# Kernel tuning notes

Hardware: AMD Instinct MI355X
Metric: run time of the kernel (lower is better)

## Reference

```python
import jax, jax.numpy as jnp
import numpy as np

L, B, T, D = 4, 32, 2048, 100


def setup_inputs() -> dict:
    key = jax.random.key(0)
    k1, k2 = jax.random.split(key)
    h = jax.random.normal(k1, (L, B, T, D), dtype=jnp.float32)
    old_h = jax.random.normal(k2, (L, B, T, D), dtype=jnp.float32)
    layer_weights = jnp.ones((L,), dtype=jnp.float32)
    class_weights = jnp.ones((D,), dtype=jnp.float32)
    return {"h": h, "old_h": old_h, "layer_weights": layer_weights, "class_weights": class_weights}


def reference(h, old_h, layer_weights, class_weights):
    # h, old_h: [L, B, T, D]. Softmax / log_softmax are over the T axis
    # (dim=-1 of h[..., c] which is [B, T]).
    logq = jax.nn.log_softmax(h, axis=2)        # student log-probs  [L,B,T,D]
    logp = jax.nn.log_softmax(old_h, axis=2)    # teacher log-probs  [L,B,T,D]
    p = jnp.exp(logp)                            # teacher probs
    # KL(p || q) per (layer, class), batchmean reduction: sum over (B,T) / B
    kl_lc = jnp.sum(p * (logp - logq), axis=(1, 2)) / jnp.float32(B)  # [L, D]
    lw = jax.nn.softmax(layer_weights)           # [L]
    cw = jax.nn.softmax(class_weights)           # [D]
    loss = jnp.einsum('l,ld,d->', lw, kl_lc, cw)
    return loss
```

## Files before the change

### kernel.cpp

```cpp
#include <hip/hip_runtime.h>

constexpr int kL = 4;
constexpr int kB = 32;
constexpr int kT = 2048;
constexpr int kD = 100;
constexpr int kD4 = kD / 4;
constexpr int kCH = 16;
constexpr int kTSUB = kT / kCH;
constexpr int kROWS = kL * kB * kD;

__global__ __launch_bounds__(256) void kl_partial(
    const float4* __restrict__ h4, const float4* __restrict__ oh4,
    float* __restrict__ wsp, float* __restrict__ wsq, float* __restrict__ ww) {
  const int lb = blockIdx.x >> 4;
  const int chunk = blockIdx.x & 15;
  const int tid = threadIdx.x;
  const int ty = tid >> 6;
  const int lane = tid & 63;
  const int half = lane / kD4;
  const int d4 = lane - half * kD4;
  const bool active = (lane < 2 * kD4);

  float4 sp = {0.f, 0.f, 0.f, 0.f};
  float4 sq = {0.f, 0.f, 0.f, 0.f};
  float4 w  = {0.f, 0.f, 0.f, 0.f};

  if (active) {
    const int row0 = chunk * kTSUB + ty * 2 + half;
    const size_t b4 = ((size_t)lb * kT + row0) * kD4 + d4;
    const float4* __restrict__ hp = h4 + b4;
    const float4* __restrict__ op = oh4 + b4;
    for (int i = 0; i < 4; ++i) {
      const float4 h0 = hp[0];
      const float4 o0 = op[0];
      const float4 h1 = hp[200];
      const float4 o1 = op[200];
      const float4 h2 = hp[400];
      const float4 o2 = op[400];
      const float4 h3 = hp[600];
      const float4 o3 = op[600];
      hp += 800; op += 800;
      {
        const float a = __expf(o0.x), b = __expf(o0.y), c = __expf(o0.z), d = __expf(o0.w);
        sp.x += a; sp.y += b; sp.z += c; sp.w += d;
        sq.x += __expf(h0.x); sq.y += __expf(h0.y); sq.z += __expf(h0.z); sq.w += __expf(h0.w);
        w.x += a * (o0.x - h0.x); w.y += b * (o0.y - h0.y);
        w.z += c * (o0.z - h0.z); w.w += d * (o0.w - h0.w);
      }
      {
        const float a = __expf(o1.x), b = __expf(o1.y), c = __expf(o1.z), d = __expf(o1.w);
        sp.x += a; sp.y += b; sp.z += c; sp.w += d;
        sq.x += __expf(h1.x); sq.y += __expf(h1.y); sq.z += __expf(h1.z); sq.w += __expf(h1.w);
        w.x += a * (o1.x - h1.x); w.y += b * (o1.y - h1.y);
        w.z += c * (o1.z - h1.z); w.w += d * (o1.w - h1.w);
      }
      {
        const float a = __expf(o2.x), b = __expf(o2.y), c = __expf(o2.z), d = __expf(o2.w);
        sp.x += a; sp.y += b; sp.z += c; sp.w += d;
        sq.x += __expf(h2.x); sq.y += __expf(h2.y); sq.z += __expf(h2.z); sq.w += __expf(h2.w);
        w.x += a * (o2.x - h2.x); w.y += b * (o2.y - h2.y);
        w.z += c * (o2.z - h2.z); w.w += d * (o2.w - h2.w);
      }
      {
        const float a = __expf(o3.x), b = __expf(o3.y), c = __expf(o3.z), d = __expf(o3.w);
        sp.x += a; sp.y += b; sp.z += c; sp.w += d;
        sq.x += __expf(h3.x); sq.y += __expf(h3.y); sq.z += __expf(h3.z); sq.w += __expf(h3.w);
        w.x += a * (o3.x - h3.x); w.y += b * (o3.y - h3.y);
        w.z += c * (o3.z - h3.z); w.w += d * (o3.w - h3.w);
      }
    }
  }

  __shared__ float red[256][12];
  {
    float* r = red[tid];
    r[0] = sp.x; r[1] = sp.y; r[2]  = sp.z; r[3]  = sp.w;
    r[4] = sq.x; r[5] = sq.y; r[6]  = sq.z; r[7]  = sq.w;
    r[8] = w.x;  r[9] = w.y;  r[10] = w.z;  r[11] = w.w;
  }
  __syncthreads();
  if (tid < kD) {
    const int dd4 = tid >> 2, j = tid & 3;
    float asp = 0.f, asq = 0.f, aw = 0.f;
#pragma unroll
    for (int g = 0; g < 4; ++g) {
#pragma unroll
      for (int hh = 0; hh < 2; ++hh) {
        const float* s = red[g * 64 + hh * kD4 + dd4];
        asp += s[j]; asq += s[4 + j]; aw += s[8 + j];
      }
    }
    const int idx = lb * kD + tid;
    atomicAdd(&wsp[idx], asp);
    atomicAdd(&wsq[idx], asq);
    atomicAdd(&ww[idx],  aw);
  }
}

__global__ __launch_bounds__(256) void kl_reduce(
    const float* __restrict__ wsp, const float* __restrict__ wsq,
    const float* __restrict__ ww, const float* __restrict__ lwin,
    const float* __restrict__ cwin, float* __restrict__ acc) {
  __shared__ float lw[kL];
  __shared__ float cw[kD];
  __shared__ float sred[256];
  const int tid = threadIdx.x;

  if (tid == 0) {
    float m = lwin[0];
    for (int i = 1; i < kL; ++i) m = fmaxf(m, lwin[i]);
    float e[kL], s = 0.f;
    for (int i = 0; i < kL; ++i) { e[i] = __expf(lwin[i] - m); s += e[i]; }
    const float inv = 1.0f / s;
    for (int i = 0; i < kL; ++i) lw[i] = e[i] * inv;
  }
  if (tid == 64) {
    float m = cwin[0];
    for (int i = 1; i < kD; ++i) m = fmaxf(m, cwin[i]);
    float s = 0.f;
    for (int i = 0; i < kD; ++i) { const float e = __expf(cwin[i] - m); cw[i] = e; s += e; }
    const float inv = 1.0f / s;
    for (int i = 0; i < kD; ++i) cw[i] *= inv;
  }
  __syncthreads();

  const int r = blockIdx.x * 256 + tid;
  const int l = r / (kB * kD);
  const int d = r % kD;
  const float spv = wsp[r], sqv = wsq[r], wv = ww[r];
  const float val = wv / spv - __logf(spv) + __logf(sqv);
  sred[tid] = lw[l] * cw[d] * val;
  __syncthreads();
  for (int s = 128; s > 0; s >>= 1) {
    if (tid < s) sred[tid] += sred[tid + s];
    __syncthreads();
  }
  if (tid == 0) atomicAdd(acc, sred[0]);
}

__global__ void kl_write(const float* __restrict__ acc, float* __restrict__ out) {
  out[0] = acc[0] / (float)kB;
}

extern "C" void kernel_launch(void* const* d_in, const int* in_sizes, int n_in,
                              void* d_out, int out_size, void* d_ws, size_t ws_size,
                              hipStream_t stream) {
  const float* h    = (const float*)d_in[0];
  const float* oh   = (const float*)d_in[1];
  const float* lwin = (const float*)d_in[2];
  const float* cwin = (const float*)d_in[3];

  float* wsp = (float*)d_ws;
  float* wsq = wsp + kROWS;
  float* ww  = wsq + kROWS;
  float* acc = ww + kROWS;
  hipMemsetAsync(d_ws, 0, ((size_t)3 * kROWS + 1) * sizeof(float), stream);

  kl_partial<<<kL * kB * kCH, 256, 0, stream>>>(
      (const float4*)h, (const float4*)oh, wsp, wsq, ww);
  kl_reduce<<<kROWS / 256, 256, 0, stream>>>(wsp, wsq, ww, lwin, cwin, acc);
  kl_write<<<1, 1, 0, stream>>>(acc, (float*)d_out);
}
```

Measured before the change: 241.8 us.

## Replace atomic accumulation and memset with deterministic per-block partials and tree reduction

When the workspace is large enough, each partial block writes its per-class sums to its own slot instead of using global atomics, which removes the memset launch and atomic contention. A per-(layer,batch) reduce kernel then sums the 16 chunks, and a small wave-shuffle kernel produces the final scalar. The streaming loop is also fully unrolled, with all loads grouped ahead of a scheduling barrier to raise memory-level parallelism. The old atomic path stays as a fallback, at the cost of a larger workspace requirement.

```diff
diff --git a/kernel.cpp b/kernel.cpp
--- a/kernel.cpp
+++ b/kernel.cpp
@@ -7,69 +7,163 @@
 constexpr int kD4 = kD / 4;
 constexpr int kCH = 16;
 constexpr int kTSUB = kT / kCH;
-constexpr int kROWS = kL * kB * kD;
-
-__global__ __launch_bounds__(256) void kl_partial(
-    const float4* __restrict__ h4, const float4* __restrict__ oh4,
-    float* __restrict__ wsp, float* __restrict__ wsq, float* __restrict__ ww) {
-  const int lb = blockIdx.x >> 4;
-  const int chunk = blockIdx.x & 15;
-  const int tid = threadIdx.x;
+constexpr int kLB = kL * kB;
+constexpr int kROWS = kLB * kD;
+constexpr int kNBLK = kLB * kCH;
+
+#define KL_PAIR(hx, ox)                                                      \
+  {                                                                          \
+    const float ea = __expf(ox.x), eb = __expf(ox.y), ec = __expf(ox.z),     \
+                ed = __expf(ox.w);                                           \
+    sp.x += ea; sp.y += eb; sp.z += ec; sp.w += ed;                          \
+    sq.x += __expf(hx.x); sq.y += __expf(hx.y);                              \
+    sq.z += __expf(hx.z); sq.w += __expf(hx.w);                              \
+    w.x += ea * (ox.x - hx.x); w.y += eb * (ox.y - hx.y);                    \
+    w.z += ec * (ox.z - hx.z); w.w += ed * (ox.w - hx.w);                    \
+  }
+
+__device__ __forceinline__ void stream_slab(const float4* __restrict__ hp,
+                                            const float4* __restrict__ op,
+                                            float4& sp, float4& sq, float4& w) {
+#pragma unroll
+  for (int i = 0; i < 4; ++i) {
+    const float4 h0 = hp[0];
+    const float4 h1 = hp[200];
+    const float4 h2 = hp[400];
+    const float4 h3 = hp[600];
+    const float4 o0 = op[0];
+    const float4 o1 = op[200];
+    const float4 o2 = op[400];
+    const float4 o3 = op[600];
+    hp += 800; op += 800;
+    __builtin_amdgcn_sched_barrier(0);
+    KL_PAIR(h0, o0)
+    KL_PAIR(h1, o1)
+    KL_PAIR(h2, o2)
+    KL_PAIR(h3, o3)
+  }
+}
+
+template <int PASS>
+__device__ __forceinline__ void partial_body(const float4* __restrict__ h4,
+                                             const float4* __restrict__ oh4,
+                                             float4& sp, float4& sq, float4& w,
+                                             int lb, int chunk, int tid) {
   const int ty = tid >> 6;
   const int lane = tid & 63;
   const int half = lane / kD4;
   const int d4 = lane - half * kD4;
   const bool active = (lane < 2 * kD4);
+  if (active) {
+    const int row0 = chunk * kTSUB + ty * 2 + half;
+    const size_t b4 = ((size_t)lb * kT + row0) * kD4 + d4;
+    stream_slab(h4 + b4, oh4 + b4, sp, sq, w);
+  }
+}
+
+__global__ __launch_bounds__(256) void kl_partial_na(
+    const float4* __restrict__ h4, const float4* __restrict__ oh4,
+    float* __restrict__ psp, float* __restrict__ psq, float* __restrict__ pw) {
+  const int lb = blockIdx.x >> 4;
+  const int chunk = blockIdx.x & 15;
+  const int tid = threadIdx.x;
 
   float4 sp = {0.f, 0.f, 0.f, 0.f};
   float4 sq = {0.f, 0.f, 0.f, 0.f};
   float4 w  = {0.f, 0.f, 0.f, 0.f};
-
-  if (active) {
-    const int row0 = chunk * kTSUB + ty * 2 + half;
-    const size_t b4 = ((size_t)lb * kT + row0) * kD4 + d4;
-    const float4* __restrict__ hp = h4 + b4;
-    const float4* __restrict__ op = oh4 + b4;
-    for (int i = 0; i < 4; ++i) {
-      const float4 h0 = hp[0];
-      const float4 o0 = op[0];
-      const float4 h1 = hp[200];
-      const float4 o1 = op[200];
-      const float4 h2 = hp[400];
-      const float4 o2 = op[400];
-      const float4 h3 = hp[600];
-      const float4 o3 = op[600];
-      hp += 800; op += 800;
-      {
-        const float a = __expf(o0.x), b = __expf(o0.y), c = __expf(o0.z), d = __expf(o0.w);
-        sp.x += a; sp.y += b; sp.z += c; sp.w += d;
-        sq.x += __expf(h0.x); sq.y += __expf(h0.y); sq.z += __expf(h0.z); sq.w += __expf(h0.w);
-        w.x += a * (o0.x - h0.x); w.y += b * (o0.y - h0.y);
-        w.z += c * (o0.z - h0.z); w.w += d * (o0.w - h0.w);
-      }
-      {
-        const float a = __expf(o1.x), b = __expf(o1.y), c = __expf(o1.z), d = __expf(o1.w);
-        sp.x += a; sp.y += b; sp.z += c; sp.w += d;
-        sq.x += __expf(h1.x); sq.y += __expf(h1.y); sq.z += __expf(h1.z); sq.w += __expf(h1.w);
-        w.x += a * (o1.x - h1.x); w.y += b * (o1.y - h1.y);
-        w.z += c * (o1.z - h1.z); w.w += d * (o1.w - h1.w);
-      }
-      {
-        const float a = __expf(o2.x), b = __expf(o2.y), c = __expf(o2.z), d = __expf(o2.w);
-        sp.x += a; sp.y += b; sp.z += c; sp.w += d;
-        sq.x += __expf(h2.x); sq.y += __expf(h2.y); sq.z += __expf(h2.z); sq.w += __expf(h2.w);
-        w.x += a * (o2.x - h2.x); w.y += b * (o2.y - h2.y);
-        w.z += c * (o2.z - h2.z); w.w += d * (o2.w - h2.w);
-      }
-      {
-        const float a = __expf(o3.x), b = __expf(o3.y), c = __expf(o3.z), d = __expf(o3.w);
-        sp.x += a; sp.y += b; sp.z += c; sp.w += d;
-        sq.x += __expf(h3.x); sq.y += __expf(h3.y); sq.z += __expf(h3.z); sq.w += __expf(h3.w);
-        w.x += a * (o3.x - h3.x); w.y += b * (o3.y - h3.y);
-        w.z += c * (o3.z - h3.z); w.w += d * (o3.w - h3.w);
+  partial_body<0>(h4, oh4, sp, sq, w, lb, chunk, tid);
+
+  __shared__ float red[256][12];
+  {
+    float* r = red[tid];
+    r[0] = sp.x; r[1] = sp.y; r[2]  = sp.z; r[3]  = sp.w;
+    r[4] = sq.x; r[5] = sq.y; r[6]  = sq.z; r[7]  = sq.w;
+    r[8] = w.x;  r[9] = w.y;  r[10] = w.z;  r[11] = w.w;
+  }
+  __syncthreads();
+  if (tid < kD) {
+    const int dd4 = tid >> 2, j = tid & 3;
+    float asp = 0.f, asq = 0.f, aw = 0.f;
+#pragma unroll
+    for (int g = 0; g < 4; ++g) {
+#pragma unroll
+      for (int hh = 0; hh < 2; ++hh) {
+        const float* s = red[g * 64 + hh * kD4 + dd4];
+        asp += s[j]; asq += s[4 + j]; aw += s[8 + j];
       }
     }
-  }
+    const int base = blockIdx.x * kD + tid;
+    psp[base] = asp;
+    psq[base] = asq;
+    pw[base]  = aw;
+  }
+}
+
+__global__ __launch_bounds__(256) void kl_reduce_na(
+    const float* __restrict__ psp, const float* __restrict__ psq,
+    const float* __restrict__ pw, const float* __restrict__ lwin,
+    const float* __restrict__ cwin, float* __restrict__ lbsum) {
+  const int lb = blockIdx.x;
+  const int tid = threadIdx.x;
+  __shared__ float lwS;
+  __shared__ float cw[kD];
+  __shared__ float sred[256];
+
+  if (tid == 0) {
+    float m = lwin[0];
+    for (int i = 1; i < kL; ++i) m = fmaxf(m, lwin[i]);
+    float e[kL], s = 0.f;
+    for (int i = 0; i < kL; ++i) { e[i] = __expf(lwin[i] - m); s += e[i]; }
+    lwS = e[lb / kB] / s;
+  }
+  if (tid == 64) {
+    float m = cwin[0];
+    for (int i = 1; i < kD; ++i) m = fmaxf(m, cwin[i]);
+    float s = 0.f;
+    for (int i = 0; i < kD; ++i) { const float e = __expf(cwin[i] - m); cw[i] = e; s += e; }
+    const float inv = 1.0f / s;
+    for (int i = 0; i < kD; ++i) cw[i] *= inv;
+  }
+  __syncthreads();
+
+  float acc = 0.f;
+  if (tid < kD) {
+    float asp = 0.f, asq = 0.f, aw = 0.f;
+#pragma unroll
+    for (int c = 0; c < kCH; ++c) {
+      const int idx = (lb * kCH + c) * kD + tid;
+      asp += psp[idx]; asq += psq[idx]; aw += pw[idx];
+    }
+    const float val = aw / asp - __logf(asp) + __logf(asq);
+    acc = lwS * cw[tid] * val * (1.0f / (float)kB);
+  }
+  sred[tid] = acc;
+  __syncthreads();
+  for (int s = 128; s > 0; s >>= 1) {
+    if (tid < s) sred[tid] += sred[tid + s];
+    __syncthreads();
+  }
+  if (tid == 0) lbsum[lb] = sred[0];
+}
+
+__global__ void kl_final(const float* __restrict__ lbsum, float* __restrict__ out) {
+  const int tid = threadIdx.x;
+  float v = lbsum[tid] + lbsum[tid + 64];
+  for (int off = 32; off > 0; off >>= 1) v += __shfl_down(v, off);
+  if (tid == 0) out[0] = v;
+}
+
+__global__ __launch_bounds__(256) void kl_partial_at(
+    const float4* __restrict__ h4, const float4* __restrict__ oh4,
+    float* __restrict__ wsp, float* __restrict__ wsq, float* __restrict__ ww) {
+  const int lb = blockIdx.x >> 4;
+  const int chunk = blockIdx.x & 15;
+  const int tid = threadIdx.x;
+
+  float4 sp = {0.f, 0.f, 0.f, 0.f};
+  float4 sq = {0.f, 0.f, 0.f, 0.f};
+  float4 w  = {0.f, 0.f, 0.f, 0.f};
+  partial_body<1>(h4, oh4, sp, sq, w, lb, chunk, tid);
 
   __shared__ float red[256][12];
   {
@@ -97,7 +191,7 @@
   }
 }
 
-__global__ __launch_bounds__(256) void kl_reduce(
+__global__ __launch_bounds__(256) void kl_reduce_at(
     const float* __restrict__ wsp, const float* __restrict__ wsq,
     const float* __restrict__ ww, const float* __restrict__ lwin,
     const float* __restrict__ cwin, float* __restrict__ acc) {
@@ -150,14 +244,25 @@
   const float* lwin = (const float*)d_in[2];
   const float* cwin = (const float*)d_in[3];
 
-  float* wsp = (float*)d_ws;
-  float* wsq = wsp + kROWS;
-  float* ww  = wsq + kROWS;
-  float* acc = ww + kROWS;
-  hipMemsetAsync(d_ws, 0, ((size_t)3 * kROWS + 1) * sizeof(float), stream);
-
-  kl_partial<<<kL * kB * kCH, 256, 0, stream>>>(
-      (const float4*)h, (const float4*)oh, wsp, wsq, ww);
-  kl_reduce<<<kROWS / 256, 256, 0, stream>>>(wsp, wsq, ww, lwin, cwin, acc);
-  kl_write<<<1, 1, 0, stream>>>(acc, (float*)d_out);
-}
+  const size_t needA = ((size_t)3 * kNBLK * kD + kLB) * sizeof(float);
+  if (ws_size >= needA) {
+    float* psp   = (float*)d_ws;
+    float* psq   = psp + (size_t)kNBLK * kD;
+    float* pw    = psq + (size_t)kNBLK * kD;
+    float* lbsum = pw  + (size_t)kNBLK * kD;
+    kl_partial_na<<<kNBLK, 256, 0, stream>>>(
+        (const float4*)h, (const float4*)oh, psp, psq, pw);
+    kl_reduce_na<<<kLB, 256, 0, stream>>>(psp, psq, pw, lwin, cwin, lbsum);
+    kl_final<<<1, 64, 0, stream>>>(lbsum, (float*)d_out);
+  } else {
+    float* wsp = (float*)d_ws;
+    float* wsq = wsp + kROWS;
+    float* ww  = wsq + kROWS;
+    float* acc = ww + kROWS;
+    hipMemsetAsync(d_ws, 0, ((size_t)3 * kROWS + 1) * sizeof(float), stream);
+    kl_partial_at<<<kNBLK, 256, 0, stream>>>(
+        (const float4*)h, (const float4*)oh, wsp, wsq, ww);
+    kl_reduce_at<<<kROWS / 256, 256, 0, stream>>>(wsp, wsq, ww, lwin, cwin, acc);
+    kl_write<<<1, 1, 0, stream>>>(acc, (float*)d_out);
+  }
+}
```

New measurement: 239.8 us. Within noise of the previous version (-0.8%).
